# Kernel optimization log

Measured on AMD Instinct MI355X. Metric: run time of the kernel, lower is better.

The kernel has to match this reference:

```python
import jax, jax.numpy as jnp
import numpy as np

D_MODEL = 512
D_STATE = 16
D_INNER = 2 * D_MODEL  # expand_factor=2
IN_CH = 256
B_SZ, H_SZ, W_SZ = 4, 32, 32


def setup_inputs() -> dict:
    key = jax.random.key(0)
    ks = jax.random.split(key, 24)
    f = jax.random.normal
    inp = {}
    inp["x_V"] = f(ks[0], (B_SZ, IN_CH, H_SZ, W_SZ), jnp.float32)
    inp["x_I"] = f(ks[1], (B_SZ, IN_CH, H_SZ, W_SZ), jnp.float32)
    # channel_reduce: 1x1 conv + BN (inference stats)
    inp["conv_red_w"] = f(ks[2], (D_MODEL, IN_CH), jnp.float32) * 0.05
    inp["bn_red_g"] = jnp.ones((D_MODEL,), jnp.float32)
    inp["bn_red_b"] = jnp.zeros((D_MODEL,), jnp.float32)
    inp["bn_red_m"] = jnp.zeros((D_MODEL,), jnp.float32)
    inp["bn_red_v"] = jnp.ones((D_MODEL,), jnp.float32)
    # channel_restore: 1x1 conv + BN
    inp["conv_res_w"] = f(ks[3], (IN_CH, D_MODEL), jnp.float32) * 0.05
    inp["bn_res_g"] = jnp.ones((IN_CH,), jnp.float32)
    inp["bn_res_b"] = jnp.zeros((IN_CH,), jnp.float32)
    inp["bn_res_m"] = jnp.zeros((IN_CH,), jnp.float32)
    inp["bn_res_v"] = jnp.ones((IN_CH,), jnp.float32)
    # lambda_predictor convs (1x1 on pooled features == linear)
    inp["lam_w1"] = f(ks[4], (D_MODEL // 4, D_MODEL * 2), jnp.float32) * 0.05
    inp["lam_b1"] = jnp.zeros((D_MODEL // 4,), jnp.float32)
    inp["lam_w2"] = f(ks[5], (2, D_MODEL // 4), jnp.float32) * 0.05
    inp["lam_b2"] = jnp.zeros((2,), jnp.float32)
    # two SimplifiedMamba2Blocks
    for i, p in enumerate(["V", "I"]):
        kk = jax.random.split(ks[6 + i], 6)
        inp[p + "_in_w"] = f(kk[0], (2 * D_INNER, D_MODEL), jnp.float32) * 0.03
        inp[p + "_out_w"] = f(kk[1], (D_MODEL, D_INNER), jnp.float32) * 0.03
        # A = -exp(A_log) in (-1, -0.05): stable decay
        inp[p + "_A_log"] = jnp.log(jax.random.uniform(kk[2], (D_INNER, D_STATE), jnp.float32, 0.05, 0.95))
        inp[p + "_B"] = f(kk[3], (D_INNER, D_STATE), jnp.float32) * 0.05
        inp[p + "_C"] = jnp.full((D_INNER, D_STATE), 0.01, jnp.float32)
        inp[p + "_ln_g"] = jnp.ones((D_MODEL,), jnp.float32)
        inp[p + "_ln_b"] = jnp.zeros((D_MODEL,), jnp.float32)
    inp["gate"] = jnp.asarray(0.1, jnp.float32)
    return inp


def _bn(x, g, b, m, v):
    # x: (B,C,H,W); inference-mode batchnorm
    return (x - m[:, None, None]) / jnp.sqrt(v[:, None, None] + 1e-5) * g[:, None, None] + b[:, None, None]


def _conv1x1(x, w):
    return jnp.einsum('bchw,oc->bohw', x, w)


def _ssm_scan(x_ssm, A, Bm, Cm, reverse):
    # x_ssm: (B,L,I); A,Bm,Cm: (I,S)
    bsz = x_ssm.shape[0]
    h0 = jnp.zeros((bsz, A.shape[0], A.shape[1]), x_ssm.dtype)

    def step(h, xt):  # xt: (B,I)
        h = jnp.clip(h * A + xt[:, :, None] * Bm, -10.0, 10.0)
        return h, jnp.einsum('bis,is->bi', h, Cm)

    _, ys = jax.lax.scan(step, h0, jnp.swapaxes(x_ssm, 0, 1), reverse=reverse)
    return jnp.swapaxes(ys, 0, 1)  # (B,L,I), in original time order


def _mamba(x, ln_g, ln_b, in_w, out_w, A_log, Bm, Cm):
    # LayerNorm
    mu = jnp.mean(x, -1, keepdims=True)
    var = jnp.mean((x - mu) ** 2, -1, keepdims=True)
    xn = (x - mu) / jnp.sqrt(var + 1e-5) * ln_g + ln_b
    xp = xn @ in_w.T  # (B,L,2*I)
    x_ssm, gate = jnp.split(xp, 2, axis=-1)
    A = jnp.clip(-jnp.exp(A_log), -10.0, -0.01)
    yf = _ssm_scan(x_ssm, A, Bm, Cm, False)
    yb = _ssm_scan(x_ssm, A, Bm, Cm, True)
    out = 0.5 * (yf + yb) * jax.nn.silu(gate)
    return out @ out_w.T


def reference(x_V, x_I, conv_red_w, bn_red_g, bn_red_b, bn_red_m, bn_red_v,
              conv_res_w, bn_res_g, bn_res_b, bn_res_m, bn_res_v,
              lam_w1, lam_b1, lam_w2, lam_b2,
              V_in_w, V_out_w, V_A_log, V_B, V_C, V_ln_g, V_ln_b,
              I_in_w, I_out_w, I_A_log, I_B, I_C, I_ln_g, I_ln_b, gate):
    B, _, H, W = x_V.shape
    xVr = jax.nn.relu(_bn(_conv1x1(x_V, conv_red_w), bn_red_g, bn_red_b, bn_red_m, bn_red_v))
    xIr = jax.nn.relu(_bn(_conv1x1(x_I, conv_red_w), bn_red_g, bn_red_b, bn_red_m, bn_red_v))
    # same spatial size -> adaptive pooling and [:B] slicing are identities
    conc = jnp.concatenate([xVr, xIr], axis=1)  # (B, 2*d_model, H, W)

    def lam(c):
        p = jnp.mean(c, axis=(2, 3))  # global avg pool -> (B, 2*d_model)
        h1 = jax.nn.relu(p @ lam_w1.T + lam_b1)
        return jax.nn.softmax(h1 @ lam_w2.T + lam_b2, axis=-1)  # (B,2)

    lamV = lam(conc)
    lamI = lam(conc)

    seq_V = jnp.swapaxes(xVr.reshape(B, D_MODEL, H * W), 1, 2)  # (B,L,D)
    seq_I = jnp.swapaxes(xIr.reshape(B, D_MODEL, H * W), 1, 2)

    outV_std = _mamba(seq_V, V_ln_g, V_ln_b, V_in_w, V_out_w, V_A_log, V_B, V_C)
    outI_std = _mamba(seq_I, I_ln_g, I_ln_b, I_in_w, I_out_w, I_A_log, I_B, I_C)
    outV_cross = _mamba(seq_V, V_ln_g, V_ln_b, V_in_w, V_out_w, V_A_log, jax.lax.stop_gradient(I_B), V_C)
    outI_cross = _mamba(seq_I, I_ln_g, I_ln_b, I_in_w, I_out_w, I_A_log, jax.lax.stop_gradient(V_B), I_C)

    outV = lamV[:, 0][:, None, None] * outV_std + lamV[:, 1][:, None, None] * outV_cross
    outI = lamI[:, 0][:, None, None] * outI_std + lamI[:, 1][:, None, None] * outI_cross

    featV = jnp.swapaxes(outV, 1, 2).reshape(B, D_MODEL, H, W)
    featI = jnp.swapaxes(outI, 1, 2).reshape(B, D_MODEL, H, W)
    featV = _bn(_conv1x1(featV, conv_res_w), bn_res_g, bn_res_b, bn_res_m, bn_res_v)
    featI = _bn(_conv1x1(featI, conv_res_w), bn_res_g, bn_res_b, bn_res_m, bn_res_v)

    g = jax.nn.sigmoid(gate)
    return (x_V + g * featV, x_I + g * featI)
```

## Files before the change

### kernel.cpp

```cpp
#include <hip/hip_runtime.h>
#include <hip/hip_bf16.h>
#include <math.h>

#define L_SZ 1024
#define DM   512
#define DI   1024
#define NS   16
#define CH   256

typedef float4 f4;
typedef __attribute__((ext_vector_type(8))) short short8;
typedef __attribute__((ext_vector_type(8))) unsigned short u16x8;
typedef __attribute__((ext_vector_type(4))) float f32x4;

__device__ __forceinline__ float bf2f(ushort u) {
    union { unsigned int i; float f; } x; x.i = ((unsigned int)u) << 16; return x.f;
}
__device__ __forceinline__ ushort f2bf(float f) {
    union { float f; unsigned int i; } x; x.f = f;
    unsigned int r = x.i + 0x7FFFu + ((x.i >> 16) & 1u);
    return (ushort)(r >> 16);
}
__device__ __forceinline__ uint pkbf(float a, float b) {
    union { __hip_bfloat162 h; uint u; } c;
    c.h = __float22bfloat162_rn(make_float2(a, b));
    return c.u;
}

#define GLOAD16(gp, lp) \
  __builtin_amdgcn_global_load_lds((const __attribute__((address_space(1))) void*)(gp), \
                                   (__attribute__((address_space(3))) void*)(lp), 16, 0, 0)

__global__ __launch_bounds__(256) void k_prep(
    const float* __restrict__ s0, const float* __restrict__ s1,
    const float* __restrict__ s2, const float* __restrict__ s3,
    const float* __restrict__ s4, const float* __restrict__ s5,
    ushort* __restrict__ d0, ushort* __restrict__ d1,
    ushort* __restrict__ d2, ushort* __restrict__ d3,
    ushort* __restrict__ d4, ushort* __restrict__ d5,
    const float* __restrict__ xv, const float* __restrict__ xi,
    ushort* __restrict__ xtv, ushort* __restrict__ xti,
    float* __restrict__ p, unsigned int* __restrict__ cnt)
{
    __shared__ float tile[32][36];
    const int bid = blockIdx.x;
    const int t = threadIdx.x;
    if (bid < 2304) {
        const float* s; ushort* d; int rel;
        if      (bid < 128)  { s = s0; d = d0; rel = bid; }
        else if (bid < 256)  { s = s1; d = d1; rel = bid - 128; }
        else if (bid < 1280) { s = s2; d = d2; rel = bid - 256; }
        else                 { s = s3; d = d3; rel = bid - 1280; }
        const int i = rel * 256 + t;
        f4 v = ((const f4*)s)[i];
        ushort4 o;
        o.x = f2bf(v.x); o.y = f2bf(v.y); o.z = f2bf(v.z); o.w = f2bf(v.w);
        ((ushort4*)d)[i] = o;
        return;
    }
    if (bid < 3328) {
        const int rel = (bid < 2816) ? bid - 2304 : bid - 2816;
        const float* wo = (bid < 2816) ? s4 : s5;
        ushort* wt      = (bid < 2816) ? d4 : d5;
        const int kt = rel & 31, dt = rel >> 5;
        const int d0_ = dt * 32, k0 = kt * 32;
        {
            int cc = t >> 3, ll4 = (t & 7) << 2;
            f4 v = *(const f4*)(wo + (size_t)(d0_ + cc) * 1024 + k0 + ll4);
            tile[cc][ll4 + 0] = v.x; tile[cc][ll4 + 1] = v.y;
            tile[cc][ll4 + 2] = v.z; tile[cc][ll4 + 3] = v.w;
        }
        __syncthreads();
        {
            int ll = t >> 3, cc4 = (t & 7) << 2;
            ushort4 o;
            o.x = f2bf(tile[cc4 + 0][ll]); o.y = f2bf(tile[cc4 + 1][ll]);
            o.z = f2bf(tile[cc4 + 2][ll]); o.w = f2bf(tile[cc4 + 3][ll]);
            *(ushort4*)(wt + (size_t)(k0 + ll) * 512 + d0_ + cc4) = o;
        }
        return;
    }
    if (bid < 5376) {
        const int rel = bid - 3328;
        const int l0 = (rel & 31) * 32, c0 = ((rel >> 5) & 7) * 32;
        const int z = rel >> 8;
        const int b = z & 3, st = z >> 2;
        const float* x = st ? xi : xv;
        ushort* xt = st ? xti : xtv;
        {
            int cc = t >> 3, ll4 = (t & 7) << 2;
            f4 v = *(const f4*)(x + ((size_t)(b * CH + c0 + cc)) * L_SZ + l0 + ll4);
            tile[cc][ll4 + 0] = v.x; tile[cc][ll4 + 1] = v.y;
            tile[cc][ll4 + 2] = v.z; tile[cc][ll4 + 3] = v.w;
        }
        __syncthreads();
        {
            int ll = t >> 3, cc4 = (t & 7) << 2;
            ushort4 o;
            o.x = f2bf(tile[cc4 + 0][ll]); o.y = f2bf(tile[cc4 + 1][ll]);
            o.z = f2bf(tile[cc4 + 2][ll]); o.w = f2bf(tile[cc4 + 3][ll]);
            *(ushort4*)(xt + ((size_t)(b * L_SZ + l0 + ll)) * CH + c0 + cc4) = o;
        }
        return;
    }
    const f4 z4 = {0.f, 0.f, 0.f, 0.f};
    ((f4*)p)[t]       = z4;
    ((f4*)p)[t + 256] = z4;
    ((f4*)p)[t + 512] = z4;
    ((f4*)p)[t + 768] = z4;
    if (t == 0) *cnt = 0u;
}

template<int MODE, int BM, int BN, int OS>
__global__ __launch_bounds__(256) void k_gemm(
    const ushort* __restrict__ A0, const ushort* __restrict__ A1,
    const ushort* __restrict__ B0, const ushort* __restrict__ B1,
    int K,
    float* __restrict__ o0, float* __restrict__ o1,
    ushort* __restrict__ ob0, ushort* __restrict__ ob1,
    ushort* __restrict__ sb0, ushort* __restrict__ sb1,
    const float* __restrict__ pg, const float* __restrict__ pb,
    const float* __restrict__ pm, const float* __restrict__ pv,
    const float* __restrict__ x0, const float* __restrict__ x1,
    const float* __restrict__ gate, float* __restrict__ pp)
{
    constexpr int MT   = BM / 32;
    constexpr int NT   = BN / 32;
    constexpr int ASEG = BM / 16;
    constexpr int NSEG = (BM + BN) / 16;
    constexpr int SPW  = NSEG / 4;
    __shared__ __align__(16) ushort Sl[2][(BM + BN) * 32];
    const int t = threadIdx.x;
    const int wv = t >> 6, lane = t & 63;
    const int n0 = blockIdx.x * BN, m0 = blockIdx.y * BM;
    const int st = blockIdx.z;
    const ushort* Ap = st ? A1 : A0;
    const ushort* Bp = st ? B1 : B0;
    const int wm = wv >> 1, wn = wv & 1;
    const int lrow = lane & 15, q = lane >> 4;
    f32x4 acc[MT][NT];
    #pragma unroll
    for (int a_ = 0; a_ < MT; ++a_)
        #pragma unroll
        for (int b_ = 0; b_ < NT; ++b_)
            acc[a_][b_] = (f32x4){0.f, 0.f, 0.f, 0.f};
    const int srow = lane >> 2;
    const int skk  = (((lane & 3) ^ ((lane >> 3) & 3)) << 3);
    const int koff = ((q ^ ((lrow >> 1) & 3)) << 3);
    #pragma unroll
    for (int s2 = 0; s2 < SPW; ++s2) {
        const int seg = wv * SPW + s2;
        const int grow = (seg < ASEG) ? (m0 + seg * 16 + srow)
                                      : (n0 + (seg - ASEG) * 16 + srow);
        const ushort* src = (seg < ASEG) ? Ap : Bp;
        GLOAD16(src + (size_t)grow * K + skk, &Sl[0][seg * 512]);
    }
    int cur = 0;
    for (int k0 = 0; k0 < K; k0 += 32) {
        if (k0 + 32 < K) {
            #pragma unroll
            for (int s2 = 0; s2 < SPW; ++s2) {
                const int seg = wv * SPW + s2;
                const int grow = (seg < ASEG) ? (m0 + seg * 16 + srow)
                                              : (n0 + (seg - ASEG) * 16 + srow);
                const ushort* src = (seg < ASEG) ? Ap : Bp;
                GLOAD16(src + (size_t)grow * K + (k0 + 32) + skk, &Sl[cur ^ 1][seg * 512]);
            }
            if constexpr (SPW == 2)      asm volatile("s_waitcnt vmcnt(2)" ::: "memory");
            else if constexpr (SPW == 3) asm volatile("s_waitcnt vmcnt(3)" ::: "memory");
            else                         asm volatile("s_waitcnt vmcnt(4)" ::: "memory");
        } else {
            asm volatile("s_waitcnt vmcnt(0)" ::: "memory");
        }
        __builtin_amdgcn_s_barrier();
        short8 af[MT], bfr[NT];
        #pragma unroll
        for (int mt = 0; mt < MT; ++mt)
            af[mt] = *(const short8*)&Sl[cur][(wm * (MT * 16) + mt * 16 + lrow) * 32 + koff];
        #pragma unroll
        for (int nt = 0; nt < NT; ++nt)
            bfr[nt] = *(const short8*)&Sl[cur][(BM + wn * (NT * 16) + nt * 16 + lrow) * 32 + koff];
        #pragma unroll
        for (int mt = 0; mt < MT; ++mt)
            #pragma unroll
            for (int nt = 0; nt < NT; ++nt) {
                if constexpr (MODE == 1)
                    acc[mt][nt] = __builtin_amdgcn_mfma_f32_16x16x32_bf16(bfr[nt], af[mt], acc[mt][nt], 0, 0, 0);
                else
                    acc[mt][nt] = __builtin_amdgcn_mfma_f32_16x16x32_bf16(af[mt], bfr[nt], acc[mt][nt], 0, 0, 0);
            }
        asm volatile("s_waitcnt lgkmcnt(0)" ::: "memory");
        __builtin_amdgcn_sched_barrier(0);
        __builtin_amdgcn_s_barrier();
        cur ^= 1;
    }
    if (MODE == 0) {
        ushort* sq = st ? ob1 : ob0;
        const int b = m0 >> 10;
        #pragma unroll
        for (int nt = 0; nt < NT; ++nt) {
            const int gn = n0 + wn * (NT * 16) + nt * 16 + lrow;
            const float s  = pg[gn] * rsqrtf(pv[gn] + 1e-5f);
            const float sh = pb[gn] - pm[gn] * s;
            float psum = 0.f;
            #pragma unroll
            for (int mt = 0; mt < MT; ++mt) {
                const int gm = m0 + wm * (MT * 16) + mt * 16 + q * 4;
                float v[4];
                #pragma unroll
                for (int r = 0; r < 4; ++r) {
                    v[r] = fmaxf(fmaf(acc[mt][nt][r], s, sh), 0.f);
                    psum += v[r];
                }
                const uint u01 = pkbf(v[0], v[1]);
                const uint u23 = pkbf(v[2], v[3]);
                ushort* bp = sq + (size_t)gm * DM + gn;
                bp[0]      = (ushort)u01;
                bp[DM]     = (ushort)(u01 >> 16);
                bp[2 * DM] = (ushort)u23;
                bp[3 * DM] = (ushort)(u23 >> 16);
            }
            psum += __shfl_xor(psum, 16, 64);
            psum += __shfl_xor(psum, 32, 64);
            if (q == 0)
                atomicAdd(pp + (b * 1024 + st * 512 + gn), psum * (1.0f / 1024.0f));
        }
    } else if (MODE == 1) {
        const bool isx = (n0 < 1024);
        ushort* xp = st ? ob1 : ob0;
        ushort* sp = st ? sb1 : sb0;
        #pragma unroll
        for (int mt = 0; mt < MT; ++mt) {
            const int gm = m0 + wm * (MT * 16) + mt * 16 + lrow;
            #pragma unroll
            for (int nt = 0; nt < NT; ++nt) {
                const int gnb = n0 + wn * (NT * 16) + nt * 16 + q * 4;
                if (isx) {
                    const uint u01 = pkbf(acc[mt][nt][0], acc[mt][nt][1]);
                    const uint u23 = pkbf(acc[mt][nt][2], acc[mt][nt][3]);
                    *(uint2*)(xp + (size_t)gm * DI + gnb) = make_uint2(u01, u23);
                } else {
                    float sv[4];
                    #pragma unroll
                    for (int r = 0; r < 4; ++r) {
                        const float v = acc[mt][nt][r];
                        sv[r] = v / (1.f + __expf(-v));
                    }
                    const uint u01 = pkbf(sv[0], sv[1]);
                    const uint u23 = pkbf(sv[2], sv[3]);
                    *(uint2*)(sp + (size_t)gm * DI + gnb - 1024) = make_uint2(u01, u23);
                }
            }
        }
    } else if (MODE == 2) {
        ushort* fp_ = st ? ob1 : ob0;
        #pragma unroll
        for (int nt = 0; nt < NT; ++nt) {
            const int gn = n0 + wn * (NT * 16) + nt * 16 + lrow;
            #pragma unroll
            for (int mt = 0; mt < MT; ++mt) {
                const int gm = m0 + wm * (MT * 16) + mt * 16 + q * 4;
                const uint u01 = pkbf(acc[mt][nt][0], acc[mt][nt][1]);
                const uint u23 = pkbf(acc[mt][nt][2], acc[mt][nt][3]);
                ushort* bp = fp_ + (size_t)gm * OS + gn;
                bp[0]      = (ushort)u01;
                bp[OS]     = (ushort)(u01 >> 16);
                bp[2 * OS] = (ushort)u23;
                bp[3 * OS] = (ushort)(u23 >> 16);
            }
        }
    } else {
        const float* xin = st ? x1 : x0;
        float* op = st ? o1 : o0;
        const float g = 1.f / (1.f + __expf(-gate[0]));
        #pragma unroll
        for (int nt = 0; nt < NT; ++nt) {
            const int gn = n0 + wn * (NT * 16) + nt * 16 + lrow;
            const float s  = pg[gn] * rsqrtf(pv[gn] + 1e-5f);
            const float sh = pb[gn] - pm[gn] * s;
            #pragma unroll
            for (int mt = 0; mt < MT; ++mt) {
                const int gmb = m0 + wm * (MT * 16) + mt * 16 + q * 4;
                const int b = gmb >> 10, l = gmb & 1023;
                const size_t off = ((size_t)(b * CH + gn)) * L_SZ + l;
                f4 xi = *(const f4*)(xin + off);
                f4 o;
                o.x = xi.x + g * fmaf(acc[mt][nt][0], s, sh);
                o.y = xi.y + g * fmaf(acc[mt][nt][1], s, sh);
                o.z = xi.z + g * fmaf(acc[mt][nt][2], s, sh);
                o.w = xi.w + g * fmaf(acc[mt][nt][3], s, sh);
                *(f4*)(op + off) = o;
            }
        }
    }
}

__global__ __launch_bounds__(256) void k_lam(
    const float* __restrict__ p, const float* __restrict__ w1,
    const float* __restrict__ b1, const float* __restrict__ w2,
    const float* __restrict__ b2, float* __restrict__ h1,
    float* __restrict__ lam, unsigned int* __restrict__ cnt)
{
    __shared__ float lsm[8];
    __shared__ unsigned int tick;
    const int t = threadIdx.x, lane = t & 63, wv = t >> 6;
    const int idx = blockIdx.x * 4 + wv;
    const int b = idx >> 7, j = idx & 127;
    const float* pb = p + b * 1024;
    const float* wr = w1 + j * 1024;
    float s = 0.f;
    #pragma unroll
    for (int k = 0; k < 16; ++k)
        s = fmaf(pb[lane + k * 64], wr[lane + k * 64], s);
    #pragma unroll
    for (int off = 1; off < 64; off <<= 1) s += __shfl_xor(s, off, 64);
    if (lane == 0) h1[idx] = fmaxf(s + b1[j], 0.f);
    __threadfence();
    __syncthreads();
    if (t == 0) tick = atomicAdd(cnt, 1u);
    __syncthreads();
    if (tick != 127u) return;
    __threadfence();
    {
        const int g32 = t >> 5, l32 = t & 31;
        const int bb = g32 >> 1, kk = g32 & 1;
        const float* hb = h1 + bb * 128;
        const float* wr2 = w2 + kk * 128;
        float ss = 0.f;
        #pragma unroll
        for (int u = 0; u < 4; ++u)
            ss = fmaf(hb[l32 + u * 32], wr2[l32 + u * 32], ss);
        #pragma unroll
        for (int off = 1; off < 32; off <<= 1) ss += __shfl_xor(ss, off, 64);
        if (l32 == 0) lsm[g32] = ss + b2[kk];
    }
    __syncthreads();
    if (t < 4) {
        const float a0 = lsm[t * 2], a1 = lsm[t * 2 + 1];
        const float m  = fmaxf(a0, a1);
        const float e0 = __expf(a0 - m), e1 = __expf(a1 - m);
        const float inv = 1.f / (e0 + e1);
        lam[t * 2 + 0] = e0 * inv;
        lam[t * 2 + 1] = e1 * inv;
    }
}

__global__ __launch_bounds__(256) void k_ln(
    const ushort* __restrict__ seq0, const ushort* __restrict__ seq1,
    const float* __restrict__ g0, const float* __restrict__ b0,
    const float* __restrict__ g1, const float* __restrict__ b1,
    ushort* __restrict__ ln0, ushort* __restrict__ ln1)
{
    const int t = threadIdx.x, lane = t & 63, wv = t >> 6;
    const int row = blockIdx.x * 4 + wv, st = blockIdx.y;
    const ushort* seq = st ? seq1 : seq0;
    const float* gg  = st ? g1 : g0;
    const float* bb  = st ? b1 : b0;
    ushort* ln = st ? ln1 : ln0;
    const u16x8 v = *(const u16x8*)(seq + (size_t)row * DM + lane * 8);
    float f[8];
    float s = 0.f, ss = 0.f;
    #pragma unroll
    for (int i = 0; i < 8; ++i) {
        f[i] = bf2f(v[i]);
        s += f[i];
        ss = fmaf(f[i], f[i], ss);
    }
    #pragma unroll
    for (int off = 1; off < 64; off <<= 1) {
        s += __shfl_xor(s, off, 64); ss += __shfl_xor(ss, off, 64);
    }
    const float mu = s * (1.f / 512.f);
    const float rstd = rsqrtf(ss * (1.f / 512.f) - mu * mu + 1e-5f);
    const f4 gv0 = *(const f4*)(gg + lane * 8);
    const f4 gv1 = *(const f4*)(gg + lane * 8 + 4);
    const f4 bv0 = *(const f4*)(bb + lane * 8);
    const f4 bv1 = *(const f4*)(bb + lane * 8 + 4);
    const float gvv[8] = {gv0.x, gv0.y, gv0.z, gv0.w, gv1.x, gv1.y, gv1.z, gv1.w};
    const float bvv[8] = {bv0.x, bv0.y, bv0.z, bv0.w, bv1.x, bv1.y, bv1.z, bv1.w};
    u16x8 o;
    #pragma unroll
    for (int i = 0; i < 8; i += 2) {
        const uint u = pkbf(fmaf((f[i]     - mu) * rstd, gvv[i],     bvv[i]),
                            fmaf((f[i + 1] - mu) * rstd, gvv[i + 1], bvv[i + 1]));
        o[i]     = (ushort)u;
        o[i + 1] = (ushort)(u >> 16);
    }
    *(u16x8*)(ln + (size_t)row * DM + lane * 8) = o;
}

__global__ __launch_bounds__(128) void k_scan(
    const ushort* __restrict__ xsV, const ushort* __restrict__ xsI,
    const ushort* __restrict__ sgV, const ushort* __restrict__ sgI,
    const float* __restrict__ VA, const float* __restrict__ VB,
    const float* __restrict__ VC, const float* __restrict__ IA,
    const float* __restrict__ IB, const float* __restrict__ IC,
    const float* __restrict__ lam,
    ushort* __restrict__ yV, ushort* __restrict__ yI)
{
    __shared__ __align__(16) ushort xf[2][16][64];
    __shared__ __align__(16) ushort xb[2][16][64];
    __shared__ __align__(16) ushort sgl[64][64];
    __shared__ ushort ybuf[4096 + 32];
#define YFB(m) (ybuf + (m) * 64)
#define YBB(m) (ybuf + 2080 + (m) * 64)
    const int t = threadIdx.x;
    const int shalf = t & 1;
    const int il = t >> 1;
    const int b = blockIdx.y;
    const int st = blockIdx.z >> 4, j = blockIdx.z & 15;
    const int c0 = blockIdx.x * 64;
    const ushort* xrow  = (st ? xsI : xsV) + (size_t)b * L_SZ * DI + c0;
    const ushort* sgrow = (st ? sgI : sgV) + (size_t)b * L_SZ * DI + c0;
    ushort* yrow        = (st ? yI  : yV ) + (size_t)b * L_SZ * DI + c0;
    const float* Alog = st ? IA : VA;
    const float* Cm   = st ? IC : VC;
    const float* Bown = st ? IB : VB;
    const float* Both = st ? VB : IB;
    const float lam0 = lam[b * 2 + 0], lam1 = lam[b * 2 + 1];
    float a[8], w[8], gf[8], gb[8];
    const int base = (c0 + il) * NS + shalf * 8;
    #pragma unroll
    for (int s = 0; s < 8; ++s) {
        a[s] = fminf(fmaxf(-__expf(Alog[base + s]), -10.f), -0.01f);
        w[s] = 0.5f * Cm[base + s] * fmaf(lam0, Bown[base + s], lam1 * Both[base + s]);
        gf[s] = 0.f; gb[s] = 0.f;
    }
    const int row0 = j << 6;
    const int srow = t >> 3;
    const int scol = (t & 7) << 3;
    const int scolS = scol ^ ((srow & 1) << 5);
    {
        int rf = row0 - 64 + srow;          rf = max(0, min(1023, rf));
        GLOAD16(xrow + (size_t)rf * DI + scol, &xf[0][srow][0]);
        int rb = row0 + 127 - srow;         rb = max(0, min(1023, rb));
        GLOAD16(xrow + (size_t)rb * DI + scol, &xb[0][srow][0]);
    }
    for (int si = 0; si < 8; ++si) {
        const int buf = si & 1;
        if (si < 7) {
            const int base2 = (si + 1) * 16;
            int rf = row0 - 64 + base2 + srow;  rf = max(0, min(1023, rf));
            GLOAD16(xrow + (size_t)rf * DI + scol, &xf[buf ^ 1][srow][0]);
            int rb = row0 + 127 - base2 - srow; rb = max(0, min(1023, rb));
            GLOAD16(xrow + (size_t)rb * DI + scol, &xb[buf ^ 1][srow][0]);
        }
        if (si == 4) {
            GLOAD16(sgrow + (size_t)(row0 + srow) * DI + scolS,      &sgl[srow][0]);
            GLOAD16(sgrow + (size_t)(row0 + 16 + srow) * DI + scolS, &sgl[16 + srow][0]);
        } else if (si == 5) {
            GLOAD16(sgrow + (size_t)(row0 + 32 + srow) * DI + scolS, &sgl[32 + srow][0]);
            GLOAD16(sgrow + (size_t)(row0 + 48 + srow) * DI + scolS, &sgl[48 + srow][0]);
        }
        if (si == 4)      asm volatile("s_waitcnt vmcnt(4)"  ::: "memory");
        else if (si == 5) asm volatile("s_waitcnt vmcnt(6)"  ::: "memory");
        else if (si < 7)  asm volatile("s_waitcnt vmcnt(2)"  ::: "memory");
        else              asm volatile("s_waitcnt vmcnt(16)" ::: "memory");
        __builtin_amdgcn_s_barrier();
        if (si == 4) {
            if (j == 0) {
                for (int s = 0; s < 8; ++s) gf[s] = 0.f;
            }
            if (j == 15) {
                for (int s = 0; s < 8; ++s) gb[s] = 0.f;
            }
        }
        if (si < 4) {
            #pragma unroll
            for (int n = 0; n < 16; ++n) {
                const float vf = bf2f(xf[buf][n][il]);
                const float vb = bf2f(xb[buf][n][il]);
                #pragma unroll
                for (int s = 0; s < 8; ++s) {
                    gf[s] = fmaf(a[s], gf[s], vf);
                    gb[s] = fmaf(a[s], gb[s], vb);
                }
            }
        } else if (si < 6) {
            const int mb = (si - 4) * 16;
            #pragma unroll
            for (int n = 0; n < 16; ++n) {
                const float vf = bf2f(xf[buf][n][il]);
                const float vb = bf2f(xb[buf][n][il]);
                float yf = 0.f, yb = 0.f;
                #pragma unroll
                for (int s = 0; s < 8; ++s) {
                    gf[s] = fmaf(a[s], gf[s], vf);
                    yf    = fmaf(gf[s], w[s], yf);
                    gb[s] = fmaf(a[s], gb[s], vb);
                    yb    = fmaf(gb[s], w[s], yb);
                }
                yf += __shfl_xor(yf, 1, 64);
                yb += __shfl_xor(yb, 1, 64);
                const int m = mb + n;
                ushort* qq = shalf ? (YBB(31 - m)) : (YFB(m));
                qq[il] = f2bf(shalf ? yb : yf);
            }
        } else {
            const int mb = (si - 6) * 16 + 32;
            #pragma unroll
            for (int n = 0; n < 16; ++n) {
                const float vf = bf2f(xf[buf][n][il]);
                const float vb = bf2f(xb[buf][n][il]);
                float yf = 0.f, yb = 0.f;
                #pragma unroll
                for (int s = 0; s < 8; ++s) {
                    gf[s] = fmaf(a[s], gf[s], vf);
                    yf    = fmaf(gf[s], w[s], yf);
                    gb[s] = fmaf(a[s], gb[s], vb);
                    yb    = fmaf(gb[s], w[s], yb);
                }
                yf += __shfl_xor(yf, 1, 64);
                yb += __shfl_xor(yb, 1, 64);
                const int m = mb + n;
                const int rF = row0 + m;
                const int rB = row0 + 63 - m;
                const int r  = shalf ? rB : rF;
                const int rr = r - row0;
                const ushort* pq = shalf ? YFB(63 - m) : YBB(m - 32);
                const float own  = shalf ? yb : yf;
                const float z = (own + bf2f(pq[il]))
                              * bf2f(sgl[rr][il ^ ((rr & 1) << 5)]);
                yrow[(size_t)r * DI + il] = f2bf(z);
            }
        }
        asm volatile("s_waitcnt lgkmcnt(0)" ::: "memory");
        __builtin_amdgcn_sched_barrier(0);
        __builtin_amdgcn_s_barrier();
    }
#undef YFB
#undef YBB
}

extern "C" void kernel_launch(void* const* d_in, const int* in_sizes, int n_in,
                              void* d_out, int out_size, void* d_ws, size_t ws_size,
                              hipStream_t stream)
{
    const float* xV       = (const float*)d_in[0];
    const float* xI       = (const float*)d_in[1];
    const float* convredw = (const float*)d_in[2];
    const float* bnredg   = (const float*)d_in[3];
    const float* bnredb   = (const float*)d_in[4];
    const float* bnredm   = (const float*)d_in[5];
    const float* bnredv   = (const float*)d_in[6];
    const float* convresw = (const float*)d_in[7];
    const float* bnresg   = (const float*)d_in[8];
    const float* bnresb   = (const float*)d_in[9];
    const float* bnresm   = (const float*)d_in[10];
    const float* bnresv   = (const float*)d_in[11];
    const float* lamw1    = (const float*)d_in[12];
    const float* lamb1    = (const float*)d_in[13];
    const float* lamw2    = (const float*)d_in[14];
    const float* lamb2    = (const float*)d_in[15];
    const float* Vinw     = (const float*)d_in[16];
    const float* Voutw    = (const float*)d_in[17];
    const float* VAlog    = (const float*)d_in[18];
    const float* VB       = (const float*)d_in[19];
    const float* VC       = (const float*)d_in[20];
    const float* Vlng     = (const float*)d_in[21];
    const float* Vlnb     = (const float*)d_in[22];
    const float* Iinw     = (const float*)d_in[23];
    const float* Ioutw    = (const float*)d_in[24];
    const float* IAlog    = (const float*)d_in[25];
    const float* IB       = (const float*)d_in[26];
    const float* IC       = (const float*)d_in[27];
    const float* Ilng     = (const float*)d_in[28];
    const float* Ilnb     = (const float*)d_in[29];
    const float* gate     = (const float*)d_in[30];

    char* W = (char*)d_ws;
    const size_t MB = 1048576;
    ushort* seqV  = (ushort*)(W + 0);
    ushort* seqI  = (ushort*)(W + 4  * MB);
    float*  p     = (float*)(W + 8 * MB);
    float*  lam   = (float*)(W + 8 * MB + 16384);
    float*  h1    = (float*)(W + 8 * MB + 32768);
    unsigned int* cnt = (unsigned int*)(W + 8 * MB + 49152);
    ushort* sgV   = (ushort*)(W + 17 * MB);
    ushort* sgI   = (ushort*)(W + 25 * MB);
    ushort* yV    = (ushort*)(W + 33 * MB);
    ushort* yI    = (ushort*)(W + 41 * MB);
    ushort* wred  = (ushort*)(W + 65 * MB);
    ushort* wres  = (ushort*)(W + 65 * MB + 262144);
    ushort* winV  = (ushort*)(W + 66 * MB);
    ushort* winI  = (ushort*)(W + 68 * MB);
    ushort* woTv  = (ushort*)(W + 70 * MB);
    ushort* woTi  = (ushort*)(W + 71 * MB);
    ushort* xtV   = (ushort*)(W + 72 * MB);
    ushort* xtI   = (ushort*)(W + 74 * MB);
    ushort* lnV   = (ushort*)(W + 76 * MB);
    ushort* lnI   = (ushort*)(W + 80 * MB);
    ushort* xsV   = (ushort*)(W + 84 * MB);
    ushort* xsI   = (ushort*)(W + 92 * MB);
    ushort* wcombV = (ushort*)(W + 100 * MB);
    ushort* wcombI = (ushort*)(W + 100 * MB + 524288);
    float*  outp  = (float*)d_out;

    k_prep<<<dim3(5377), 256, 0, stream>>>(
        convredw, convresw, Vinw, Iinw, Voutw, Ioutw,
        wred, wres, winV, winI, woTv, woTi,
        xV, xI, xtV, xtI, p, cnt);
    k_gemm<2, 64, 64, 1024><<<dim3(16, 4, 2), 256, 0, stream>>>(
        wres, wres, woTv, woTi, 512,
        nullptr, nullptr, wcombV, wcombI, nullptr, nullptr,
        nullptr, nullptr, nullptr, nullptr, nullptr, nullptr, nullptr, nullptr);
    k_gemm<0, 128, 64, 512><<<dim3(8, 32, 2), 256, 0, stream>>>(xtV, xtI, wred, wred, 256,
        nullptr, nullptr, seqV, seqI, nullptr, nullptr,
        bnredg, bnredb, bnredm, bnredv, nullptr, nullptr, nullptr, p);
    k_lam<<<128, 256, 0, stream>>>(p, lamw1, lamb1, lamw2, lamb2, h1, lam, cnt);
    k_ln<<<dim3(1024, 2), 256, 0, stream>>>(seqV, seqI, Vlng, Vlnb, Ilng, Ilnb, lnV, lnI);
    k_gemm<1, 128, 128, 512><<<dim3(16, 32, 2), 256, 0, stream>>>(lnV, lnI, winV, winI, 512,
        nullptr, nullptr, xsV, xsI, sgV, sgI,
        nullptr, nullptr, nullptr, nullptr, nullptr, nullptr, nullptr, nullptr);
    k_scan<<<dim3(16, 4, 32), 128, 0, stream>>>(xsV, xsI, sgV, sgI,
        VAlog, VB, VC, IAlog, IB, IC, lam, yV, yI);
    k_gemm<3, 64, 64, 512><<<dim3(4, 64, 2), 256, 0, stream>>>(yV, yI, wcombV, wcombI, 1024,
        outp, outp + 1048576, nullptr, nullptr, nullptr, nullptr,
        bnresg, bnresb, bnresm, bnresv, xV, xI, gate, nullptr);
}
```

Measured before the change: 241.7 us.

## Triple-buffer scan staging, stash partial outputs in registers, drop trailing barriers

Restructures the k_scan pipeline to use three LDS stage buffers, so the end-of-iteration wait and barrier can go. The backward/forward partial results for the combine step now live in a fully unrolled per-thread register array instead of an LDS ybuf. The sigmoid gate is read straight from global memory instead of being staged through LDS. Launch bounds request 4 blocks per SIMD. The cost is higher register pressure from the 32-entry stash and scattered 2-byte global gate reads in the final phase.

```diff
diff --git a/kernel.cpp b/kernel.cpp
--- a/kernel.cpp
+++ b/kernel.cpp
@@ -389,7 +389,7 @@
     *(u16x8*)(ln + (size_t)row * DM + lane * 8) = o;
 }
 
-__global__ __launch_bounds__(128) void k_scan(
+__global__ __launch_bounds__(128, 4) void k_scan(
     const ushort* __restrict__ xsV, const ushort* __restrict__ xsI,
     const ushort* __restrict__ sgV, const ushort* __restrict__ sgI,
     const float* __restrict__ VA, const float* __restrict__ VB,
@@ -398,12 +398,8 @@
     const float* __restrict__ lam,
     ushort* __restrict__ yV, ushort* __restrict__ yI)
 {
-    __shared__ __align__(16) ushort xf[2][16][64];
-    __shared__ __align__(16) ushort xb[2][16][64];
-    __shared__ __align__(16) ushort sgl[64][64];
-    __shared__ ushort ybuf[4096 + 32];
-#define YFB(m) (ybuf + (m) * 64)
-#define YBB(m) (ybuf + 2080 + (m) * 64)
+    __shared__ __align__(16) ushort xf[3][16][64];
+    __shared__ __align__(16) ushort xb[3][16][64];
     const int t = threadIdx.x;
     const int shalf = t & 1;
     const int il = t >> 1;
@@ -429,107 +425,90 @@
     const int row0 = j << 6;
     const int srow = t >> 3;
     const int scol = (t & 7) << 3;
-    const int scolS = scol ^ ((srow & 1) << 5);
-    {
-        int rf = row0 - 64 + srow;          rf = max(0, min(1023, rf));
-        GLOAD16(xrow + (size_t)rf * DI + scol, &xf[0][srow][0]);
-        int rb = row0 + 127 - srow;         rb = max(0, min(1023, rb));
-        GLOAD16(xrow + (size_t)rb * DI + scol, &xb[0][srow][0]);
-    }
-    for (int si = 0; si < 8; ++si) {
-        const int buf = si & 1;
-        if (si < 7) {
-            const int base2 = (si + 1) * 16;
-            int rf = row0 - 64 + base2 + srow;  rf = max(0, min(1023, rf));
-            GLOAD16(xrow + (size_t)rf * DI + scol, &xf[buf ^ 1][srow][0]);
-            int rb = row0 + 127 - base2 - srow; rb = max(0, min(1023, rb));
-            GLOAD16(xrow + (size_t)rb * DI + scol, &xb[buf ^ 1][srow][0]);
-        }
-        if (si == 4) {
-            GLOAD16(sgrow + (size_t)(row0 + srow) * DI + scolS,      &sgl[srow][0]);
-            GLOAD16(sgrow + (size_t)(row0 + 16 + srow) * DI + scolS, &sgl[16 + srow][0]);
-        } else if (si == 5) {
-            GLOAD16(sgrow + (size_t)(row0 + 32 + srow) * DI + scolS, &sgl[32 + srow][0]);
-            GLOAD16(sgrow + (size_t)(row0 + 48 + srow) * DI + scolS, &sgl[48 + srow][0]);
-        }
-        if (si == 4)      asm volatile("s_waitcnt vmcnt(4)"  ::: "memory");
-        else if (si == 5) asm volatile("s_waitcnt vmcnt(6)"  ::: "memory");
-        else if (si < 7)  asm volatile("s_waitcnt vmcnt(2)"  ::: "memory");
-        else              asm volatile("s_waitcnt vmcnt(16)" ::: "memory");
-        __builtin_amdgcn_s_barrier();
-        if (si == 4) {
-            if (j == 0) {
-                for (int s = 0; s < 8; ++s) gf[s] = 0.f;
-            }
-            if (j == 15) {
-                for (int s = 0; s < 8; ++s) gb[s] = 0.f;
-            }
-        }
-        if (si < 4) {
-            #pragma unroll
-            for (int n = 0; n < 16; ++n) {
-                const float vf = bf2f(xf[buf][n][il]);
-                const float vb = bf2f(xb[buf][n][il]);
-                #pragma unroll
-                for (int s = 0; s < 8; ++s) {
-                    gf[s] = fmaf(a[s], gf[s], vf);
-                    gb[s] = fmaf(a[s], gb[s], vb);
-                }
-            }
-        } else if (si < 6) {
-            const int mb = (si - 4) * 16;
-            #pragma unroll
-            for (int n = 0; n < 16; ++n) {
-                const float vf = bf2f(xf[buf][n][il]);
-                const float vb = bf2f(xb[buf][n][il]);
-                float yf = 0.f, yb = 0.f;
-                #pragma unroll
-                for (int s = 0; s < 8; ++s) {
-                    gf[s] = fmaf(a[s], gf[s], vf);
-                    yf    = fmaf(gf[s], w[s], yf);
-                    gb[s] = fmaf(a[s], gb[s], vb);
-                    yb    = fmaf(gb[s], w[s], yb);
-                }
-                yf += __shfl_xor(yf, 1, 64);
-                yb += __shfl_xor(yb, 1, 64);
-                const int m = mb + n;
-                ushort* qq = shalf ? (YBB(31 - m)) : (YFB(m));
-                qq[il] = f2bf(shalf ? yb : yf);
-            }
-        } else {
-            const int mb = (si - 6) * 16 + 32;
-            #pragma unroll
-            for (int n = 0; n < 16; ++n) {
-                const float vf = bf2f(xf[buf][n][il]);
-                const float vb = bf2f(xb[buf][n][il]);
-                float yf = 0.f, yb = 0.f;
-                #pragma unroll
-                for (int s = 0; s < 8; ++s) {
-                    gf[s] = fmaf(a[s], gf[s], vf);
-                    yf    = fmaf(gf[s], w[s], yf);
-                    gb[s] = fmaf(a[s], gb[s], vb);
-                    yb    = fmaf(gb[s], w[s], yb);
-                }
-                yf += __shfl_xor(yf, 1, 64);
-                yb += __shfl_xor(yb, 1, 64);
-                const int m = mb + n;
-                const int rF = row0 + m;
-                const int rB = row0 + 63 - m;
-                const int r  = shalf ? rB : rF;
-                const int rr = r - row0;
-                const ushort* pq = shalf ? YFB(63 - m) : YBB(m - 32);
-                const float own  = shalf ? yb : yf;
-                const float z = (own + bf2f(pq[il]))
-                              * bf2f(sgl[rr][il ^ ((rr & 1) << 5)]);
-                yrow[(size_t)r * DI + il] = f2bf(z);
-            }
-        }
-        asm volatile("s_waitcnt lgkmcnt(0)" ::: "memory");
-        __builtin_amdgcn_sched_barrier(0);
-        __builtin_amdgcn_s_barrier();
-    }
-#undef YFB
-#undef YBB
+    ushort stash[32];
+
+#define STAGE(PH, BUF) do { \
+    int rf_ = row0 - 64 + (PH) * 16 + srow; rf_ = max(0, min(1023, rf_)); \
+    GLOAD16(xrow + (size_t)rf_ * DI + scol, &xf[BUF][srow][0]); \
+    int rb_ = row0 + 127 - (PH) * 16 - srow; rb_ = max(0, min(1023, rb_)); \
+    GLOAD16(xrow + (size_t)rb_ * DI + scol, &xb[BUF][srow][0]); \
+} while (0)
+
+#define WBODY(BUF) \
+    _Pragma("unroll") \
+    for (int n = 0; n < 16; ++n) { \
+        const float vf = bf2f(xf[BUF][n][il]); \
+        const float vb = bf2f(xb[BUF][n][il]); \
+        _Pragma("unroll") \
+        for (int s = 0; s < 8; ++s) { \
+            gf[s] = fmaf(a[s], gf[s], vf); \
+            gb[s] = fmaf(a[s], gb[s], vb); \
+        } \
+    }
+
+#define SBODY(MB, BUF) \
+    _Pragma("unroll") \
+    for (int n = 0; n < 16; ++n) { \
+        const float vf = bf2f(xf[BUF][n][il]); \
+        const float vb = bf2f(xb[BUF][n][il]); \
+        float yf = 0.f, yb = 0.f; \
+        _Pragma("unroll") \
+        for (int s = 0; s < 8; ++s) { \
+            gf[s] = fmaf(a[s], gf[s], vf); yf = fmaf(gf[s], w[s], yf); \
+            gb[s] = fmaf(a[s], gb[s], vb); yb = fmaf(gb[s], w[s], yb); \
+        } \
+        yf += __shfl_xor(yf, 1, 64); \
+        yb += __shfl_xor(yb, 1, 64); \
+        stash[(MB) + n] = f2bf(shalf ? yf : yb); \
+    }
+
+#define FBODY(MB, BUF) \
+    _Pragma("unroll") \
+    for (int n = 0; n < 16; ++n) { \
+        const float vf = bf2f(xf[BUF][n][il]); \
+        const float vb = bf2f(xb[BUF][n][il]); \
+        float yf = 0.f, yb = 0.f; \
+        _Pragma("unroll") \
+        for (int s = 0; s < 8; ++s) { \
+            gf[s] = fmaf(a[s], gf[s], vf); yf = fmaf(gf[s], w[s], yf); \
+            gb[s] = fmaf(a[s], gb[s], vb); yb = fmaf(gb[s], w[s], yb); \
+        } \
+        yf += __shfl_xor(yf, 1, 64); \
+        yb += __shfl_xor(yb, 1, 64); \
+        const int m_ = (MB) + n; \
+        const int r_ = row0 + (shalf ? (63 - m_) : m_); \
+        const float own_ = shalf ? yb : yf; \
+        const float z_ = (own_ + bf2f(stash[63 - m_])) \
+                       * bf2f(sgrow[(size_t)r_ * DI + il]); \
+        yrow[(size_t)r_ * DI + il] = f2bf(z_); \
+    }
+
+#define VMW(N) asm volatile("s_waitcnt vmcnt(" #N ")" ::: "memory")
+
+    STAGE(0, 0);
+    STAGE(1, 1); VMW(2); __builtin_amdgcn_s_barrier(); WBODY(0);
+    STAGE(2, 2); VMW(2); __builtin_amdgcn_s_barrier(); WBODY(1);
+    STAGE(3, 0); VMW(2); __builtin_amdgcn_s_barrier(); WBODY(2);
+    STAGE(4, 1); VMW(2); __builtin_amdgcn_s_barrier(); WBODY(0);
+    STAGE(5, 2); VMW(2); __builtin_amdgcn_s_barrier();
+    if (j == 0) {
+        #pragma unroll
+        for (int s = 0; s < 8; ++s) gf[s] = 0.f;
+    }
+    if (j == 15) {
+        #pragma unroll
+        for (int s = 0; s < 8; ++s) gb[s] = 0.f;
+    }
+    SBODY(0, 1);
+    STAGE(6, 0); VMW(2); __builtin_amdgcn_s_barrier(); SBODY(16, 2);
+    STAGE(7, 1); VMW(2); __builtin_amdgcn_s_barrier(); FBODY(32, 0);
+    VMW(32);             __builtin_amdgcn_s_barrier(); FBODY(48, 1);
+
+#undef STAGE
+#undef WBODY
+#undef SBODY
+#undef FBODY
+#undef VMW
 }
 
 extern "C" void kernel_launch(void* const* d_in, const int* in_sizes, int n_in,
```

After: 243.8 us. Within noise of the previous version (+0.8%).
